# Optimization experiments

Measured on AMD Instinct MI355X. Metric: run time of the kernel, lower is better.

The kernel has to match this reference:

```python
import jax, jax.numpy as jnp
import numpy as np

B, S, E, L = 8, 2048, 512, 128


def setup_inputs() -> dict:
    key = jax.random.key(0)
    k1, k2 = jax.random.split(key)
    embeddings = jax.random.normal(k1, (B, S, E), dtype=jnp.float32)
    means = jax.random.normal(k2, (L, E), dtype=jnp.float32)
    var = jnp.ones((E,), dtype=jnp.float32)  # default init: requires_grad=False, ones
    return {"embeddings": embeddings, "means": means, "var": var}


def reference(embeddings, means, var):
    # Diagonal-Gaussian log-density per (token, label):
    #   log_density - 0.5 * sum_e (means[l,e] - emb[b,s,e])^2 / var[e]
    # Rewritten as GEMM + per-row/per-label norms (avoids [B,S,L,E] intermediate).
    n_embed = embeddings.shape[-1]
    factor = -n_embed / 2.0 * (np.log(2.0) + np.log(np.pi))
    # After init_params: log_density = factor - 0.5 * sum(log var); var=ones -> factor.
    log_density = factor - 0.5 * jnp.sum(jnp.log(var))
    inv_var = 1.0 / var  # [E]
    e2 = jnp.einsum('bse,e->bs', embeddings * embeddings, inv_var)      # [B,S]
    m2 = jnp.einsum('le,e->l', means * means, inv_var)                  # [L]
    cross = jnp.einsum('bse,le->bsl', embeddings, means * inv_var)      # [B,S,L]
    sq_mahalanobis = e2[..., None] + m2[None, None, :] - 2.0 * cross    # [B,S,L]
    return log_density - 0.5 * sq_mahalanobis
```

## Files before the change

### kernel.cpp

```cpp
#include <hip/hip_runtime.h>
#include <math.h>

#define BDIM 8
#define SDIM 2048
#define EDIM 512
#define LDIM 128
#define MTOT (BDIM * SDIM)
#define TM 16
#define BK 64
#define NCH (EDIM / BK)
#define LSTR 72

typedef __attribute__((ext_vector_type(8))) short s8v;
typedef __attribute__((ext_vector_type(4))) short s4v;
typedef __attribute__((ext_vector_type(4))) float f4v;

__device__ __forceinline__ unsigned short f2bf(float x) {
    union { float f; unsigned u; } c; c.f = x;
    return (unsigned short)((c.u + 0x7fffu + ((c.u >> 16) & 1u)) >> 16);
}

__global__ __launch_bounds__(64) void gs_prep(
    const float* __restrict__ means, const float* __restrict__ var,
    unsigned short* __restrict__ BF, float* __restrict__ m2,
    float* __restrict__ ivbuf, float* __restrict__ coef)
{
    const int l = blockIdx.x;
    const int t = threadIdx.x;
    const int e0 = t * 8;

    float mv[8], iv[8];
    const float* mrow = means + l * EDIM + e0;
#pragma unroll
    for (int i = 0; i < 8; ++i) { mv[i] = mrow[i]; iv[i] = 1.0f / var[e0 + i]; }

    float part = 0.0f;
    s8v pr;
#pragma unroll
    for (int i = 0; i < 8; ++i) {
        float p = mv[i] * iv[i];
        pr[i] = (short)f2bf(p);
        part += mv[i] * p;
    }
    const int ct = l >> 4, fr = l & 15;
    const int kt = t >> 2, kg = t & 3;
    *(s8v*)(BF + (((kt * 8 + ct) * 64) + kg * 16 + fr) * 8) = pr;

#pragma unroll
    for (int off = 32; off > 0; off >>= 1) part += __shfl_down(part, off, 64);
    if (t == 0) m2[l] = part;

    if (l == 0) {
#pragma unroll
        for (int i = 0; i < 8; ++i) ivbuf[e0 + i] = iv[i];
        float ld = 0.0f;
#pragma unroll
        for (int i = 0; i < 8; ++i) ld += logf(var[e0 + i]);
#pragma unroll
        for (int off = 32; off > 0; off >>= 1) ld += __shfl_down(ld, off, 64);
        if (t == 0) {
            const float factor = -(float)EDIM * 0.5f * 1.8378770664093453f;
            *coef = factor - 0.5f * ld;
        }
    }
}

__global__ __launch_bounds__(256) void gs_main(
    const float* __restrict__ emb, const unsigned short* __restrict__ BF,
    const float* __restrict__ m2, const float* __restrict__ ivbuf,
    const float* __restrict__ coef, float* __restrict__ out)
{
    __shared__ __align__(16) unsigned short Alds[2][TM][LSTR];
    __shared__ float e2s[TM];

    const int t    = threadIdx.x;
    const int lane = t & 63;
    const int wave = t >> 6;
    const int m0   = blockIdx.x * TM;

    const int arow = t >> 4;
    const int kq   = (t & 15) * 4;

    const int fr = lane & 15;
    const int kg = lane >> 4;

    const float* embp = emb + (m0 + arow) * EDIM + kq;
    const unsigned short* bfp = BF + (wave * 2 * 64 + lane) * 8;

    f4v acc0 = (f4v)0.0f, acc1 = (f4v)0.0f;
    float e2acc = 0.0f;

    f4v a_cur  = *(const f4v*)(embp);
    f4v iv_cur = *(const f4v*)(ivbuf + kq);
    s8v b00 = *(const s8v*)(bfp);
    s8v b01 = *(const s8v*)(bfp + 512);
    s8v b10 = *(const s8v*)(bfp + 4096);
    s8v b11 = *(const s8v*)(bfp + 4608);

#pragma unroll
    for (int kc = 0; kc < NCH; ++kc) {
        s4v a4;
#pragma unroll
        for (int i = 0; i < 4; ++i) {
            a4[i] = (short)f2bf(a_cur[i]);
            e2acc += a_cur[i] * a_cur[i] * iv_cur[i];
        }
        *(s4v*)&Alds[kc & 1][arow][kq] = a4;

        f4v a_nxt, iv_nxt;
        s8v nb00, nb01, nb10, nb11;
        if (kc + 1 < NCH) {
            a_nxt  = *(const f4v*)(embp + (kc + 1) * BK);
            iv_nxt = *(const f4v*)(ivbuf + (kc + 1) * BK + kq);
            const unsigned short* bp = bfp + (kc + 1) * 8192;
            nb00 = *(const s8v*)(bp);
            nb01 = *(const s8v*)(bp + 512);
            nb10 = *(const s8v*)(bp + 4096);
            nb11 = *(const s8v*)(bp + 4608);
        }
        __syncthreads();

        s8v af0 = *(const s8v*)&Alds[kc & 1][fr][kg * 8];
        s8v af1 = *(const s8v*)&Alds[kc & 1][fr][32 + kg * 8];
        acc0 = __builtin_amdgcn_mfma_f32_16x16x32_bf16(af0, b00, acc0, 0, 0, 0);
        acc1 = __builtin_amdgcn_mfma_f32_16x16x32_bf16(af0, b01, acc1, 0, 0, 0);
        acc0 = __builtin_amdgcn_mfma_f32_16x16x32_bf16(af1, b10, acc0, 0, 0, 0);
        acc1 = __builtin_amdgcn_mfma_f32_16x16x32_bf16(af1, b11, acc1, 0, 0, 0);

        if (kc + 1 < NCH) {
            a_cur = a_nxt; iv_cur = iv_nxt;
            b00 = nb00; b01 = nb01; b10 = nb10; b11 = nb11;
        }
    }

#pragma unroll
    for (int off = 8; off > 0; off >>= 1) e2acc += __shfl_down(e2acc, off, 16);
    if ((t & 15) == 0) e2s[arow] = e2acc;
    __syncthreads();

    const float cf  = *coef;
    const int   n0  = wave * 32 + fr;
    const float cm0 = cf - 0.5f * m2[n0];
    const float cm1 = cf - 0.5f * m2[n0 + 16];
    float* orow = out + m0 * LDIM;
#pragma unroll
    for (int r = 0; r < 4; ++r) {
        const int row = kg * 4 + r;
        const float eh = 0.5f * e2s[row];
        orow[row * LDIM + n0]      = acc0[r] + cm0 - eh;
        orow[row * LDIM + n0 + 16] = acc1[r] + cm1 - eh;
    }
}

extern "C" void kernel_launch(void* const* d_in, const int* in_sizes, int n_in,
                              void* d_out, int out_size, void* d_ws, size_t ws_size,
                              hipStream_t stream) {
    const float* emb   = (const float*)d_in[0];
    const float* means = (const float*)d_in[1];
    const float* var   = (const float*)d_in[2];
    float* out = (float*)d_out;

    char* ws = (char*)d_ws;
    unsigned short* BF = (unsigned short*)ws;
    float* m2    = (float*)(ws + 131072);
    float* ivbuf = (float*)(ws + 131584);
    float* coef  = (float*)(ws + 133632);

    gs_prep<<<LDIM, 64, 0, stream>>>(means, var, BF, m2, ivbuf, coef);
    gs_main<<<MTOT / TM, 256, 0, stream>>>(emb, BF, m2, ivbuf, coef, out);
}
```

Baseline: 83.44 us.

## Load A fragments directly from global into MFMA layout, drop LDS staging

Each wave now reads its own 16x8 fp32 slices of the embedding rows straight from global memory in MFMA operand layout. This removes the shared-memory A tile, the per-chunk __syncthreads, and the software double-buffered prefetch. The squared-norm reduction now uses cross-lane shuffles instead of LDS. In exchange, each of the four waves in a block re-reads and re-converts the same 16 embedding rows, giving four times the global/L2 traffic and bf16 conversion work for A. The loads are also less coalesced, strided by row across lanes.

```diff
diff --git a/kernel.cpp b/kernel.cpp
--- a/kernel.cpp
+++ b/kernel.cpp
@@ -7,12 +7,8 @@
 #define LDIM 128
 #define MTOT (BDIM * SDIM)
 #define TM 16
-#define BK 64
-#define NCH (EDIM / BK)
-#define LSTR 72
 
 typedef __attribute__((ext_vector_type(8))) short s8v;
-typedef __attribute__((ext_vector_type(4))) short s4v;
 typedef __attribute__((ext_vector_type(4))) float f4v;
 
 __device__ __forceinline__ unsigned short f2bf(float x) {
@@ -70,73 +66,47 @@
     const float* __restrict__ m2, const float* __restrict__ ivbuf,
     const float* __restrict__ coef, float* __restrict__ out)
 {
-    __shared__ __align__(16) unsigned short Alds[2][TM][LSTR];
-    __shared__ float e2s[TM];
-
     const int t    = threadIdx.x;
     const int lane = t & 63;
     const int wave = t >> 6;
     const int m0   = blockIdx.x * TM;
 
-    const int arow = t >> 4;
-    const int kq   = (t & 15) * 4;
-
     const int fr = lane & 15;
     const int kg = lane >> 4;
 
-    const float* embp = emb + (m0 + arow) * EDIM + kq;
+    const float* ap  = emb + (m0 + fr) * EDIM + kg * 8;
+    const float* ivp = ivbuf + kg * 8;
     const unsigned short* bfp = BF + (wave * 2 * 64 + lane) * 8;
 
     f4v acc0 = (f4v)0.0f, acc1 = (f4v)0.0f;
     float e2acc = 0.0f;
 
-    f4v a_cur  = *(const f4v*)(embp);
-    f4v iv_cur = *(const f4v*)(ivbuf + kq);
-    s8v b00 = *(const s8v*)(bfp);
-    s8v b01 = *(const s8v*)(bfp + 512);
-    s8v b10 = *(const s8v*)(bfp + 4096);
-    s8v b11 = *(const s8v*)(bfp + 4608);
+#pragma unroll 4
+    for (int c = 0; c < 16; ++c) {
+        f4v x0 = *(const f4v*)(ap + c * 32);
+        f4v x1 = *(const f4v*)(ap + c * 32 + 4);
+        f4v v0 = *(const f4v*)(ivp + c * 32);
+        f4v v1 = *(const f4v*)(ivp + c * 32 + 4);
+        s8v b0 = *(const s8v*)(bfp + c * 4096);
+        s8v b1 = *(const s8v*)(bfp + c * 4096 + 512);
 
-#pragma unroll
-    for (int kc = 0; kc < NCH; ++kc) {
-        s4v a4;
+        s8v a8;
 #pragma unroll
         for (int i = 0; i < 4; ++i) {
-            a4[i] = (short)f2bf(a_cur[i]);
-            e2acc += a_cur[i] * a_cur[i] * iv_cur[i];
+            a8[i] = (short)f2bf(x0[i]);
+            e2acc += x0[i] * x0[i] * v0[i];
         }
-        *(s4v*)&Alds[kc & 1][arow][kq] = a4;
-
-        f4v a_nxt, iv_nxt;
-        s8v nb00, nb01, nb10, nb11;
-        if (kc + 1 < NCH) {
-            a_nxt  = *(const f4v*)(embp + (kc + 1) * BK);
-            iv_nxt = *(const f4v*)(ivbuf + (kc + 1) * BK + kq);
-            const unsigned short* bp = bfp + (kc + 1) * 8192;
-            nb00 = *(const s8v*)(bp);
-            nb01 = *(const s8v*)(bp + 512);
-            nb10 = *(const s8v*)(bp + 4096);
-            nb11 = *(const s8v*)(bp + 4608);
+#pragma unroll
+        for (int i = 0; i < 4; ++i) {
+            a8[4 + i] = (short)f2bf(x1[i]);
+            e2acc += x1[i] * x1[i] * v1[i];
         }
-        __syncthreads();
-
-        s8v af0 = *(const s8v*)&Alds[kc & 1][fr][kg * 8];
-        s8v af1 = *(const s8v*)&Alds[kc & 1][fr][32 + kg * 8];
-        acc0 = __builtin_amdgcn_mfma_f32_16x16x32_bf16(af0, b00, acc0, 0, 0, 0);
-        acc1 = __builtin_amdgcn_mfma_f32_16x16x32_bf16(af0, b01, acc1, 0, 0, 0);
-        acc0 = __builtin_amdgcn_mfma_f32_16x16x32_bf16(af1, b10, acc0, 0, 0, 0);
-        acc1 = __builtin_amdgcn_mfma_f32_16x16x32_bf16(af1, b11, acc1, 0, 0, 0);
-
-        if (kc + 1 < NCH) {
-            a_cur = a_nxt; iv_cur = iv_nxt;
-            b00 = nb00; b01 = nb01; b10 = nb10; b11 = nb11;
-        }
+        acc0 = __builtin_amdgcn_mfma_f32_16x16x32_bf16(a8, b0, acc0, 0, 0, 0);
+        acc1 = __builtin_amdgcn_mfma_f32_16x16x32_bf16(a8, b1, acc1, 0, 0, 0);
     }
 
-#pragma unroll
-    for (int off = 8; off > 0; off >>= 1) e2acc += __shfl_down(e2acc, off, 16);
-    if ((t & 15) == 0) e2s[arow] = e2acc;
-    __syncthreads();
+    e2acc += __shfl_xor(e2acc, 16, 64);
+    e2acc += __shfl_xor(e2acc, 32, 64);
 
     const float cf  = *coef;
     const int   n0  = wave * 32 + fr;
@@ -146,7 +116,7 @@
 #pragma unroll
     for (int r = 0; r < 4; ++r) {
         const int row = kg * 4 + r;
-        const float eh = 0.5f * e2s[row];
+        const float eh = 0.5f * __shfl(e2acc, row, 64);
         orow[row * LDIM + n0]      = acc0[r] + cm0 - eh;
         orow[row * LDIM + n0 + 16] = acc1[r] + cm1 - eh;
     }
```

After: 96.96 us. +16.2%, slower.
